# Kernel optimization log

Measured on AMD Instinct MI355X. Metric: run time of the kernel, lower is better.

## Reference

```python
import jax, jax.numpy as jnp
import numpy as np
import math

D_MODEL = 1024
N_HEAD = 16
D_HEAD = D_MODEL // N_HEAD


def setup_inputs() -> dict:
    key = jax.random.key(0)
    k0, k1, k2, k3, k4 = jax.random.split(key, 5)
    B, N = 4, 2048
    inp = jax.random.normal(k0, (B, N, D_MODEL), dtype=jnp.float32)
    # causal mask: True = keep (masked_fill on ~mask)
    mask = jnp.tril(jnp.ones((N, N), dtype=bool))
    # qkv_proj Linear(d_model, 3*d_model); output Linear(d_model, d_model)
    s_in = 1.0 / math.sqrt(D_MODEL)
    W_qkv = jax.random.uniform(k1, (D_MODEL, 3 * D_MODEL), jnp.float32, -s_in, s_in)
    b_qkv = jax.random.uniform(k2, (3 * D_MODEL,), jnp.float32, -s_in, s_in)
    W_out = jax.random.uniform(k3, (D_MODEL, D_MODEL), jnp.float32, -s_in, s_in)
    b_out = jax.random.uniform(k4, (D_MODEL,), jnp.float32, -s_in, s_in)
    return {"input": inp, "W_qkv": W_qkv, "b_qkv": b_qkv,
            "W_out": W_out, "b_out": b_out, "mask": mask}


def reference(input, W_qkv, b_qkv, W_out, b_out, mask):
    B, N, d = input.shape
    qkv = input @ W_qkv + b_qkv                       # [B,N,3d]  (dropout=eval no-op)
    q, k, v = jnp.split(qkv, 3, axis=-1)
    # [B,N,H,Dh] -> [B,H,N,Dh]
    q = q.reshape(B, N, N_HEAD, D_HEAD).transpose(0, 2, 1, 3)
    k = k.reshape(B, N, N_HEAD, D_HEAD).transpose(0, 2, 1, 3)
    v = v.reshape(B, N, N_HEAD, D_HEAD).transpose(0, 2, 1, 3)
    scale = 1.0 / math.sqrt(D_HEAD)
    scores = jnp.einsum('bhqd,bhkd->bhqk', q, k) * scale   # [B,H,N,N]
    scores = jnp.where(mask, scores, -jnp.inf)
    attn = jax.nn.softmax(scores, axis=-1)
    out = jnp.einsum('bhqk,bhkd->bhqd', attn, v)           # [B,H,N,Dh]
    out = out.transpose(0, 2, 1, 3).reshape(B, N, d)       # concat heads
    return out @ W_out + b_out
```

## Files before the change

### kernel.cpp

```cpp
#include <hip/hip_runtime.h>
#include <hip/hip_bf16.h>

typedef unsigned short u16;
typedef unsigned u32;
typedef __attribute__((ext_vector_type(4))) unsigned short u16x4;
typedef __attribute__((ext_vector_type(8))) unsigned short u16x8;
typedef __attribute__((ext_vector_type(4))) unsigned u32x4;
typedef __attribute__((ext_vector_type(8))) __bf16 bf16x8;
typedef __attribute__((ext_vector_type(4))) float f32x4;

typedef __attribute__((address_space(1))) void as1v;
typedef __attribute__((address_space(3))) void as3v;

#define MFMA16(a, b, c) __builtin_amdgcn_mfma_f32_16x16x32_bf16(a, b, c, 0, 0, 0)

#if __has_builtin(__builtin_amdgcn_permlane16_swap) && __has_builtin(__builtin_amdgcn_permlane32_swap)
#define HAVE_PERMLANE_SWAP 1
#else
#define HAVE_PERMLANE_SWAP 0
#endif

__device__ __forceinline__ u16 f2bf(float f) {
    unsigned u = __builtin_bit_cast(unsigned, f);
    u += 0x7fffu + ((u >> 16) & 1u);
    return (u16)(u >> 16);
}

__device__ __forceinline__ u32 pkbf(float lo, float hi) {
    u32 r;
    asm("v_cvt_pk_bf16_f32 %0, %1, %2" : "=v"(r) : "v"(lo), "v"(hi));
    return r;
}

__device__ __forceinline__ void gload16(const void* g, void* l) {
    __builtin_amdgcn_global_load_lds((as1v*)g, (as3v*)l, 16, 0, 0);
}

__device__ __forceinline__ float redmax_cross(float v) {
#if HAVE_PERMLANE_SWAP
    u32 xu = __builtin_bit_cast(u32, v);
    auto r16 = __builtin_amdgcn_permlane16_swap(xu, xu, false, false);
    float a = fmaxf(__builtin_bit_cast(float, (u32)r16[0]),
                    __builtin_bit_cast(float, (u32)r16[1]));
    u32 au = __builtin_bit_cast(u32, a);
    auto r32 = __builtin_amdgcn_permlane32_swap(au, au, false, false);
    return fmaxf(__builtin_bit_cast(float, (u32)r32[0]),
                 __builtin_bit_cast(float, (u32)r32[1]));
#else
    v = fmaxf(v, __shfl_xor(v, 16, 64));
    return fmaxf(v, __shfl_xor(v, 32, 64));
#endif
}

__device__ __forceinline__ float redsum_cross(float v) {
#if HAVE_PERMLANE_SWAP
    u32 xu = __builtin_bit_cast(u32, v);
    auto r16 = __builtin_amdgcn_permlane16_swap(xu, xu, false, false);
    float a = __builtin_bit_cast(float, (u32)r16[0]) +
              __builtin_bit_cast(float, (u32)r16[1]);
    u32 au = __builtin_bit_cast(u32, a);
    auto r32 = __builtin_amdgcn_permlane32_swap(au, au, false, false);
    return __builtin_bit_cast(float, (u32)r32[0]) +
           __builtin_bit_cast(float, (u32)r32[1]);
#else
    v += __shfl_xor(v, 16, 64);
    return v + __shfl_xor(v, 32, 64);
#endif
}

__global__ void convert_f32_bf16(const float* __restrict__ in, u16* __restrict__ out, int n4) {
    int i = blockIdx.x * blockDim.x + threadIdx.x;
    if (i < n4) {
        float4 v = *(const float4*)&in[(size_t)i * 4];
        u16x4 o;
        o.x = f2bf(v.x); o.y = f2bf(v.y); o.z = f2bf(v.z); o.w = f2bf(v.w);
        *(u16x4*)&out[(size_t)i * 4] = o;
    }
}

__global__ void transpose_convert(const float* __restrict__ in, u16* __restrict__ out, int R, int C) {
    __shared__ float tl[64][65];
    const int rb = blockIdx.x, cb = blockIdx.y;
    const int tid = threadIdx.x;
    for (int it = 0; it < 4; ++it) {
        int lin = (tid + it * 256) * 4;
        int r = lin >> 6, c = lin & 63;
        float4 v = *(const float4*)&in[(size_t)(rb * 64 + r) * C + cb * 64 + c];
        tl[r][c + 0] = v.x; tl[r][c + 1] = v.y; tl[r][c + 2] = v.z; tl[r][c + 3] = v.w;
    }
    __syncthreads();
    for (int it = 0; it < 4; ++it) {
        int lin = (tid + it * 256) * 4;
        int oc = lin >> 6, orr = lin & 63;
        u16x4 o;
        o.x = f2bf(tl[orr + 0][oc]);
        o.y = f2bf(tl[orr + 1][oc]);
        o.z = f2bf(tl[orr + 2][oc]);
        o.w = f2bf(tl[orr + 3][oc]);
        *(u16x4*)&out[(size_t)(cb * 64 + oc) * R + rb * 64 + orr] = o;
    }
}

__global__ void transpose_v(const u16* __restrict__ vbuf, u16* __restrict__ vtb) {
    __shared__ u16 tl[64][65];
    const int nb = blockIdx.x, bh = blockIdx.y;
    const int tid = threadIdx.x;
    for (int it = 0; it < 2; ++it) {
        int lin = (tid + it * 256) * 8;
        int nl = lin >> 6, dh = lin & 63;
        u16x8 v = *(const u16x8*)&vbuf[((size_t)bh * 2048 + nb * 64 + nl) * 64 + dh];
#pragma unroll
        for (int j = 0; j < 8; ++j) tl[dh + j][nl] = v[j];
    }
    __syncthreads();
    for (int it = 0; it < 2; ++it) {
        int lin = (tid + it * 256) * 8;
        int dh = lin >> 6, nl = lin & 63;
        u16x8 o;
#pragma unroll
        for (int j = 0; j < 8; ++j) o[j] = tl[dh][nl + j];
        *(u16x8*)&vtb[((size_t)bh * 64 + dh) * 2048 + nb * 64 + nl] = o;
    }
}

__global__ __launch_bounds__(512, 2) void gemm256_qkv(
    const u16* __restrict__ A, const u16* __restrict__ Bt, const float* __restrict__ bias,
    u16* __restrict__ qb, u16* __restrict__ kb, u16* __restrict__ vb) {
    constexpr int K = 1024;
    constexpr int NT = 32;
    __shared__ u16 ldsu[65536];

    const int bid = blockIdx.x;
    const int swz = (bid & 7) * 48 + (bid >> 3);
    const int bm = swz / 12, bn = swz % 12;

    const int tid = threadIdx.x, wid = tid >> 6, lane = tid & 63;
    const int wr = wid >> 2, wc = wid & 3;
    const int l15 = lane & 15, lhi = lane >> 4;

    const int sslot = (lane & 7) ^ (lane >> 3);
    const int kcol = (sslot & 3) * 8;
    const int mloc = (lane >> 3) * 2 + (sslot >> 2);

    const u16* Arow[2];
    const u16* Brow[2];
#pragma unroll
    for (int li = 0; li < 2; ++li) {
        int sg = wid * 2 + li;
        int m = sg * 16 + mloc;
        Arow[li] = A + (size_t)(bm * 256 + m) * K + kcol;
        Brow[li] = Bt + (size_t)(bn * 256 + m) * K + kcol;
    }

    auto stageA = [&](int buf, int t) {
#pragma unroll
        for (int li = 0; li < 2; ++li) {
            int sg = wid * 2 + li;
            gload16(Arow[li] + t * 32, (char*)ldsu + buf * 32768 + sg * 1024);
        }
    };
    auto stageB = [&](int buf, int t) {
#pragma unroll
        for (int li = 0; li < 2; ++li) {
            int sg = wid * 2 + li;
            gload16(Brow[li] + t * 32, (char*)ldsu + buf * 32768 + 16384 + sg * 1024);
        }
    };

    const int rslot = ((l15 & 1) * 4 + lhi) ^ ((l15 >> 1) & 7);
    const int fragoff = (l15 >> 1) * 64 + rslot * 8;

    f32x4 acc[8][4];
#pragma unroll
    for (int i = 0; i < 8; ++i)
#pragma unroll
        for (int j = 0; j < 4; ++j) acc[i][j] = (f32x4){0.f, 0.f, 0.f, 0.f};

    auto doTile = [&](int cur, int tstage, bool dostage) {
        const u16* Ab = ldsu + cur * 16384 + wr * 4096 + fragoff;
        const u16* Bb = ldsu + cur * 16384 + 8192 + wc * 2048 + fragoff;
        bf16x8 af[8], b0, b1;
#pragma unroll
        for (int mf = 0; mf < 8; ++mf) af[mf] = *(const bf16x8*)(Ab + mf * 512);
        b0 = *(const bf16x8*)(Bb);
        b1 = *(const bf16x8*)(Bb + 512);
        if (dostage) stageA(tstage & 3, tstage);
        __builtin_amdgcn_s_setprio(1);
#pragma unroll
        for (int mf = 0; mf < 8; ++mf) {
            acc[mf][0] = MFMA16(af[mf], b0, acc[mf][0]);
            acc[mf][1] = MFMA16(af[mf], b1, acc[mf][1]);
        }
        __builtin_amdgcn_s_setprio(0);
        b0 = *(const bf16x8*)(Bb + 1024);
        b1 = *(const bf16x8*)(Bb + 1536);
        if (dostage) stageB(tstage & 3, tstage);
        __builtin_amdgcn_s_setprio(1);
#pragma unroll
        for (int mf = 0; mf < 8; ++mf) {
            acc[mf][2] = MFMA16(af[mf], b0, acc[mf][2]);
            acc[mf][3] = MFMA16(af[mf], b1, acc[mf][3]);
        }
        __builtin_amdgcn_s_setprio(0);
    };

    stageA(0, 0); stageB(0, 0);
    stageA(1, 1); stageB(1, 1);
    stageA(2, 2); stageB(2, 2);
    asm volatile("s_waitcnt vmcnt(8)" ::: "memory");
    __builtin_amdgcn_s_barrier();
    __builtin_amdgcn_sched_barrier(0);

    for (int t = 0; t < NT - 3; ++t) {
        doTile(t & 3, t + 3, true);
        asm volatile("s_waitcnt vmcnt(8)" ::: "memory");
        __builtin_amdgcn_s_barrier();
        __builtin_amdgcn_sched_barrier(0);
    }
    doTile((NT - 3) & 3, 0, false);
    asm volatile("s_waitcnt vmcnt(4)" ::: "memory");
    __builtin_amdgcn_s_barrier();
    __builtin_amdgcn_sched_barrier(0);
    doTile((NT - 2) & 3, 0, false);
    asm volatile("s_waitcnt vmcnt(0)" ::: "memory");
    __builtin_amdgcn_s_barrier();
    __builtin_amdgcn_sched_barrier(0);
    doTile((NT - 1) & 3, 0, false);

    const int bnbase = bn * 256 + wc * 64;
#pragma unroll
    for (int nf = 0; nf < 4; ++nf) {
        int cg = bnbase + nf * 16 + l15;
        float bv = bias[cg];
        int which = cg >> 10, rem = cg & 1023;
        u16* dst = (which == 0) ? qb : (which == 1) ? kb : vb;
        float qs = (which == 0) ? 0.18033688011112042f : 1.0f;
        size_t colterm = (size_t)(rem >> 6) * 131072 + (size_t)(rem & 63);
#pragma unroll
        for (int mf = 0; mf < 8; ++mf) {
            int rgb = bm * 256 + wr * 128 + mf * 16 + lhi * 4;
            size_t rowterm = (size_t)(rgb >> 11) * 2097152 + (size_t)(rgb & 2047) * 64;
#pragma unroll
            for (int v = 0; v < 4; ++v) {
                float val = (acc[mf][nf][v] + bv) * qs;
                dst[rowterm + (size_t)v * 64 + colterm] = f2bf(val);
            }
        }
    }
}

__global__ __launch_bounds__(512, 2) void gemm256_out(
    const u16* __restrict__ A, const u16* __restrict__ Bt, const float* __restrict__ bias,
    float* __restrict__ outf) {
    constexpr int K = 1024;
    constexpr int NT = 32;
    __shared__ u16 ldsu[49152];

    const int bid = blockIdx.x;
    const int swz = (bid & 7) * 32 + (bid >> 3);
    const int bm = swz >> 3, bn = swz & 7;

    const int tid = threadIdx.x, wid = tid >> 6, lane = tid & 63;
    const int wr = wid >> 2, wc = wid & 3;
    const int l15 = lane & 15, lhi = lane >> 4;

    const int sslot = (lane & 7) ^ (lane >> 3);
    const int kcol = (sslot & 3) * 8;
    const int mloc = (lane >> 3) * 2 + (sslot >> 2);

    const u16* Arow[2];
#pragma unroll
    for (int li = 0; li < 2; ++li) {
        int sg = wid * 2 + li;
        Arow[li] = A + (size_t)(bm * 256 + sg * 16 + mloc) * K + kcol;
    }
    const u16* Brow = Bt + (size_t)(bn * 128 + wid * 16 + mloc) * K + kcol;

    auto stageA = [&](int buf, int t) {
#pragma unroll
        for (int li = 0; li < 2; ++li) {
            int sg = wid * 2 + li;
            gload16(Arow[li] + t * 32, (char*)ldsu + buf * 24576 + sg * 1024);
        }
    };
    auto stageB = [&](int buf, int t) {
        gload16(Brow + t * 32, (char*)ldsu + buf * 24576 + 16384 + wid * 1024);
    };

    const int rslot = ((l15 & 1) * 4 + lhi) ^ ((l15 >> 1) & 7);
    const int fragoff = (l15 >> 1) * 64 + rslot * 8;

    f32x4 acc[8][2];
#pragma unroll
    for (int i = 0; i < 8; ++i) {
        acc[i][0] = (f32x4){0.f, 0.f, 0.f, 0.f};
        acc[i][1] = (f32x4){0.f, 0.f, 0.f, 0.f};
    }

    auto doTile = [&](int cur, int tstage, bool dostage) {
        const u16* Ab = ldsu + cur * 12288 + wr * 4096 + fragoff;
        const u16* Bb = ldsu + cur * 12288 + 8192 + wc * 1024 + fragoff;
        bf16x8 af[8], b0, b1;
#pragma unroll
        for (int mf = 0; mf < 8; ++mf) af[mf] = *(const bf16x8*)(Ab + mf * 512);
        b0 = *(const bf16x8*)(Bb);
        b1 = *(const bf16x8*)(Bb + 512);
        if (dostage) stageA(tstage & 3, tstage);
        __builtin_amdgcn_s_setprio(1);
#pragma unroll
        for (int mf = 0; mf < 8; ++mf) acc[mf][0] = MFMA16(af[mf], b0, acc[mf][0]);
        __builtin_amdgcn_s_setprio(0);
        if (dostage) stageB(tstage & 3, tstage);
        __builtin_amdgcn_s_setprio(1);
#pragma unroll
        for (int mf = 0; mf < 8; ++mf) acc[mf][1] = MFMA16(af[mf], b1, acc[mf][1]);
        __builtin_amdgcn_s_setprio(0);
    };

    stageA(0, 0); stageB(0, 0);
    stageA(1, 1); stageB(1, 1);
    stageA(2, 2); stageB(2, 2);
    asm volatile("s_waitcnt vmcnt(6)" ::: "memory");
    __builtin_amdgcn_s_barrier();
    __builtin_amdgcn_sched_barrier(0);

    for (int t = 0; t < NT - 3; ++t) {
        doTile(t & 3, t + 3, true);
        asm volatile("s_waitcnt vmcnt(6)" ::: "memory");
        __builtin_amdgcn_s_barrier();
        __builtin_amdgcn_sched_barrier(0);
    }
    doTile((NT - 3) & 3, 0, false);
    asm volatile("s_waitcnt vmcnt(3)" ::: "memory");
    __builtin_amdgcn_s_barrier();
    __builtin_amdgcn_sched_barrier(0);
    doTile((NT - 2) & 3, 0, false);
    asm volatile("s_waitcnt vmcnt(0)" ::: "memory");
    __builtin_amdgcn_s_barrier();
    __builtin_amdgcn_sched_barrier(0);
    doTile((NT - 1) & 3, 0, false);

#pragma unroll
    for (int nf = 0; nf < 2; ++nf) {
        int cg = bn * 128 + wc * 32 + nf * 16 + l15;
        float bv = bias[cg];
#pragma unroll
        for (int mf = 0; mf < 8; ++mf) {
            int rgb = bm * 256 + wr * 128 + mf * 16 + lhi * 4;
#pragma unroll
            for (int v = 0; v < 4; ++v)
                outf[(size_t)(rgb + v) * 1024 + cg] = acc[mf][nf][v] + bv;
        }
    }
}

__global__ __launch_bounds__(256, 4) void attn_kernel(
    const u16* __restrict__ qbuf, const u16* __restrict__ kbuf,
    const u16* __restrict__ vtb, u16* __restrict__ obuf) {
    __shared__ u16 Kl[2][64 * 64];
    __shared__ u16 Vl[2][64 * 64];
    const int bid = blockIdx.x;
    const int rr = bid >> 8;
    const int pp = (bid >> 6) & 3;
    const int c = (rr & 1) ? (((rr >> 1) << 2) + pp)
                           : (15 - ((rr >> 1) << 2) - pp);
    const int bh = ((bid & 7) << 3) + ((bid >> 3) & 7);
    const int b = bh >> 4, h = bh & 15;
    const int tid = threadIdx.x, wid = tid >> 6, lane = tid & 63;
    const int l15 = lane & 15, lhi = lane >> 4;
    const int q0 = c * 128 + wid * 32;
    const int ntW = 2 * c + (wid >> 1) + 1;
    const int ntmax = 2 * c + 2;

    auto loadQ = [&](int qbase, bf16x8* dst) {
        const u16* qp = qbuf + ((size_t)bh * 2048 + qbase + l15) * 64 + lhi * 8;
        dst[0] = *(const bf16x8*)(qp);
        dst[1] = *(const bf16x8*)(qp + 32);
    };
    bf16x8 qf0[2], qf1[2];
    loadQ(q0, qf0); loadQ(q0 + 16, qf1);

    float m0 = -1e30f, l0 = 0.f, m1 = -1e30f, l1 = 0.f;
    f32x4 o0[4], o1[4];
#pragma unroll
    for (int d = 0; d < 4; ++d) {
        o0[d] = (f32x4){0.f, 0.f, 0.f, 0.f};
        o1[d] = (f32x4){0.f, 0.f, 0.f, 0.f};
    }

    const int srow = lane >> 3;
    const int scolb = ((lane & 7) * 16) ^ (srow << 4);

    auto stage = [&](int buf, int t) {
        const int kbase = t * 64;
#pragma unroll
        for (int s = 0; s < 2; ++s) {
            int sg = wid * 2 + s;
            int row = sg * 8 + srow;
            const u16* gk = kbuf + ((size_t)bh * 2048 + kbase + row) * 64 + (scolb >> 1);
            gload16(gk, (char*)Kl[buf] + sg * 1024);
            const u16* gv = vtb + ((size_t)bh * 64 + row) * 2048 + kbase + (scolb >> 1);
            gload16(gv, (char*)Vl[buf] + sg * 1024);
        }
    };

    auto smax = [&](f32x4* s, int qg0, int t, float& m, float& l, f32x4* oa, u32* pw) {
        const int qg = qg0 + l15;
        if (64 * t + 63 > qg0) {
#pragma unroll
            for (int kb4 = 0; kb4 < 4; ++kb4)
#pragma unroll
                for (int v = 0; v < 4; ++v) {
                    int kg = 64 * t + kb4 * 16 + lhi * 4 + v;
                    if (kg > qg) s[kb4][v] = -1e30f;
                }
        }
        float pm = fmaxf(fmaxf(fmaxf(s[0][0], s[0][1]), fmaxf(s[0][2], s[0][3])),
                         fmaxf(fmaxf(s[1][0], s[1][1]), fmaxf(s[1][2], s[1][3])));
        pm = fmaxf(pm, fmaxf(fmaxf(fmaxf(s[2][0], s[2][1]), fmaxf(s[2][2], s[2][3])),
                             fmaxf(fmaxf(s[3][0], s[3][1]), fmaxf(s[3][2], s[3][3]))));
        pm = redmax_cross(pm);
        if (!__all(pm <= m + 8.f)) {
            float nm = fmaxf(m, pm);
            float f = exp2f(m - nm);
            m = nm;
            l *= f;
#pragma unroll
            for (int d = 0; d < 4; ++d)
#pragma unroll
                for (int v = 0; v < 4; ++v) oa[d][v] *= f;
        }
        float rs = 0.f;
#pragma unroll
        for (int kb4 = 0; kb4 < 4; ++kb4)
#pragma unroll
            for (int v = 0; v < 4; ++v) {
                float e = exp2f(s[kb4][v] - m);
                s[kb4][v] = e;
                rs += e;
            }
        l += redsum_cross(rs);
        pw[0] = pkbf(s[0][0], s[0][1]); pw[1] = pkbf(s[0][2], s[0][3]);
        pw[2] = pkbf(s[1][0], s[1][1]); pw[3] = pkbf(s[1][2], s[1][3]);
        pw[4] = pkbf(s[2][0], s[2][1]); pw[5] = pkbf(s[2][2], s[2][3]);
        pw[6] = pkbf(s[3][0], s[3][1]); pw[7] = pkbf(s[3][2], s[3][3]);
    };

    auto computeChunk = [&](const char* Kb, const char* Vb, int t) {
        f32x4 s0[4], s1[4];
        __builtin_amdgcn_s_setprio(1);
#pragma unroll
        for (int kb4 = 0; kb4 < 4; ++kb4) {
            const int r = kb4 * 16 + l15;
            const int sw = (r & 7) << 4;
            const int rowb = r * 128;
            bf16x8 kf0 = *(const bf16x8*)(Kb + rowb + ((lhi * 16) ^ sw));
            bf16x8 kf1 = *(const bf16x8*)(Kb + rowb + ((64 + lhi * 16) ^ sw));
            f32x4 a0 = (f32x4){0.f, 0.f, 0.f, 0.f};
            a0 = MFMA16(kf0, qf0[0], a0);
            a0 = MFMA16(kf1, qf0[1], a0);
            s0[kb4] = a0;
            f32x4 a1 = (f32x4){0.f, 0.f, 0.f, 0.f};
            a1 = MFMA16(kf0, qf1[0], a1);
            a1 = MFMA16(kf1, qf1[1], a1);
            s1[kb4] = a1;
        }
        __builtin_amdgcn_s_setprio(0);
        u32 pw0[8], pw1[8];
        smax(s0, q0, t, m0, l0, o0, pw0);
        smax(s1, q0 + 16, t, m1, l1, o1, pw1);
        __builtin_amdgcn_s_setprio(1);
#pragma unroll
        for (int ks = 0; ks < 2; ++ks) {
            bf16x8 pb0 = __builtin_bit_cast(bf16x8,
                (u32x4){pw0[ks * 4 + 0], pw0[ks * 4 + 1], pw0[ks * 4 + 2], pw0[ks * 4 + 3]});
            bf16x8 pb1 = __builtin_bit_cast(bf16x8,
                (u32x4){pw1[ks * 4 + 0], pw1[ks * 4 + 1], pw1[ks * 4 + 2], pw1[ks * 4 + 3]});
#pragma unroll
            for (int dhb = 0; dhb < 4; ++dhb) {
                const int r = dhb * 16 + l15;
                const int sw = (r & 7) << 4;
                u16x4 v0 = *(const u16x4*)(Vb + r * 128 + ((ks * 64 + 8 * lhi) ^ sw));
                u16x4 v1 = *(const u16x4*)(Vb + r * 128 + ((ks * 64 + 32 + 8 * lhi) ^ sw));
                u16x8 vv = {v0[0], v0[1], v0[2], v0[3], v1[0], v1[1], v1[2], v1[3]};
                bf16x8 vf = __builtin_bit_cast(bf16x8, vv);
                o0[dhb] = MFMA16(vf, pb0, o0[dhb]);
                o1[dhb] = MFMA16(vf, pb1, o1[dhb]);
            }
        }
        __builtin_amdgcn_s_setprio(0);
    };

    stage(0, 0);
    int t = 0;
    for (;;) {
        __syncthreads();
        if (t + 1 < ntmax) stage(1, t + 1);
        if (t < ntW) computeChunk((const char*)Kl[0], (const char*)Vl[0], t);
        if (++t == ntmax) break;
        __syncthreads();
        if (t + 1 < ntmax) stage(0, t + 1);
        if (t < ntW) computeChunk((const char*)Kl[1], (const char*)Vl[1], t);
        if (++t == ntmax) break;
    }

    auto epi = [&](int qg0, float l, const f32x4* oa) {
        const float rl = 1.f / l;
        const int q = qg0 + l15;
        const size_t rowoff = ((size_t)b * 2048 + q) * 1024 + h * 64;
#pragma unroll
        for (int dhb = 0; dhb < 4; ++dhb) {
            u16x4 w;
#pragma unroll
            for (int v = 0; v < 4; ++v) w[v] = f2bf(oa[dhb][v] * rl);
            *(u16x4*)&obuf[rowoff + dhb * 16 + lhi * 4] = w;
        }
    };
    epi(q0, l0, o0);
    epi(q0 + 16, l1, o1);
}

extern "C" void kernel_launch(void* const* d_in, const int* in_sizes, int n_in,
                              void* d_out, int out_size, void* d_ws, size_t ws_size,
                              hipStream_t stream) {
    const float* inp   = (const float*)d_in[0];
    const float* W_qkv = (const float*)d_in[1];
    const float* b_qkv = (const float*)d_in[2];
    const float* W_out = (const float*)d_in[3];
    const float* b_out = (const float*)d_in[4];
    float* out = (float*)d_out;

    u16* xb   = (u16*)d_ws;
    u16* wqt  = xb + 8388608;
    u16* wot  = wqt + 3145728;
    u16* qbuf = wot + 1048576;
    u16* kbuf = qbuf + 8388608;
    u16* vbuf = kbuf + 8388608;
    u16* vtb  = vbuf + 8388608;
    u16* obuf = vtb + 8388608;

    convert_f32_bf16<<<8192, 256, 0, stream>>>(inp, xb, 2097152);
    transpose_convert<<<dim3(16, 48), 256, 0, stream>>>(W_qkv, wqt, 1024, 3072);
    transpose_convert<<<dim3(16, 16), 256, 0, stream>>>(W_out, wot, 1024, 1024);
    gemm256_qkv<<<384, 512, 0, stream>>>(xb, wqt, b_qkv, qbuf, kbuf, vbuf);
    transpose_v<<<dim3(32, 64), 256, 0, stream>>>(vbuf, vtb);
    attn_kernel<<<1024, 256, 0, stream>>>(qbuf, kbuf, vtb, obuf);
    gemm256_out<<<256, 512, 0, stream>>>(obuf, wot, b_out, out);
}
```

Baseline: 185.3 us.

## Shrink QKV GEMM tile to 256x128 and stage epilogue through LDS for coalesced stores

The QKV projection GEMM now uses 256x128 output tiles instead of 256x256, doubling the grid to 768 blocks and cutting LDS per block and accumulator registers per wave. The epilogue first writes biased, scaled bf16 results into a swizzled LDS scratch area, then emits 16-byte vector stores to the head-major Q/K/V buffers instead of scattered 2-byte stores. The aim is better occupancy and CU balance plus coalesced output writes. The cost is more A-tile reloads from global memory and lower MFMA work per loaded B fragment.

```diff
diff --git a/kernel.cpp b/kernel.cpp
--- a/kernel.cpp
+++ b/kernel.cpp
@@ -128,11 +128,11 @@
     u16* __restrict__ qb, u16* __restrict__ kb, u16* __restrict__ vb) {
     constexpr int K = 1024;
     constexpr int NT = 32;
-    __shared__ u16 ldsu[65536];
+    __shared__ u16 ldsu[49152];
 
     const int bid = blockIdx.x;
-    const int swz = (bid & 7) * 48 + (bid >> 3);
-    const int bm = swz / 12, bn = swz % 12;
+    const int swz = (bid & 7) * 96 + (bid >> 3);
+    const int bm = swz / 24, bn = swz % 24;
 
     const int tid = threadIdx.x, wid = tid >> 6, lane = tid & 63;
     const int wr = wid >> 2, wc = wid & 3;
@@ -143,42 +143,37 @@
     const int mloc = (lane >> 3) * 2 + (sslot >> 2);
 
     const u16* Arow[2];
-    const u16* Brow[2];
 #pragma unroll
     for (int li = 0; li < 2; ++li) {
         int sg = wid * 2 + li;
-        int m = sg * 16 + mloc;
-        Arow[li] = A + (size_t)(bm * 256 + m) * K + kcol;
-        Brow[li] = Bt + (size_t)(bn * 256 + m) * K + kcol;
-    }
+        Arow[li] = A + (size_t)(bm * 256 + sg * 16 + mloc) * K + kcol;
+    }
+    const u16* Brow = Bt + (size_t)(bn * 128 + wid * 16 + mloc) * K + kcol;
 
     auto stageA = [&](int buf, int t) {
 #pragma unroll
         for (int li = 0; li < 2; ++li) {
             int sg = wid * 2 + li;
-            gload16(Arow[li] + t * 32, (char*)ldsu + buf * 32768 + sg * 1024);
+            gload16(Arow[li] + t * 32, (char*)ldsu + buf * 24576 + sg * 1024);
         }
     };
     auto stageB = [&](int buf, int t) {
-#pragma unroll
-        for (int li = 0; li < 2; ++li) {
-            int sg = wid * 2 + li;
-            gload16(Brow[li] + t * 32, (char*)ldsu + buf * 32768 + 16384 + sg * 1024);
-        }
+        gload16(Brow + t * 32, (char*)ldsu + buf * 24576 + 16384 + wid * 1024);
     };
 
     const int rslot = ((l15 & 1) * 4 + lhi) ^ ((l15 >> 1) & 7);
     const int fragoff = (l15 >> 1) * 64 + rslot * 8;
 
-    f32x4 acc[8][4];
-#pragma unroll
-    for (int i = 0; i < 8; ++i)
-#pragma unroll
-        for (int j = 0; j < 4; ++j) acc[i][j] = (f32x4){0.f, 0.f, 0.f, 0.f};
+    f32x4 acc[8][2];
+#pragma unroll
+    for (int i = 0; i < 8; ++i) {
+        acc[i][0] = (f32x4){0.f, 0.f, 0.f, 0.f};
+        acc[i][1] = (f32x4){0.f, 0.f, 0.f, 0.f};
+    }
 
     auto doTile = [&](int cur, int tstage, bool dostage) {
-        const u16* Ab = ldsu + cur * 16384 + wr * 4096 + fragoff;
-        const u16* Bb = ldsu + cur * 16384 + 8192 + wc * 2048 + fragoff;
+        const u16* Ab = ldsu + cur * 12288 + wr * 4096 + fragoff;
+        const u16* Bb = ldsu + cur * 12288 + 8192 + wc * 1024 + fragoff;
         bf16x8 af[8], b0, b1;
 #pragma unroll
         for (int mf = 0; mf < 8; ++mf) af[mf] = *(const bf16x8*)(Ab + mf * 512);
@@ -187,38 +182,30 @@
         if (dostage) stageA(tstage & 3, tstage);
         __builtin_amdgcn_s_setprio(1);
 #pragma unroll
-        for (int mf = 0; mf < 8; ++mf) {
-            acc[mf][0] = MFMA16(af[mf], b0, acc[mf][0]);
-            acc[mf][1] = MFMA16(af[mf], b1, acc[mf][1]);
-        }
+        for (int mf = 0; mf < 8; ++mf) acc[mf][0] = MFMA16(af[mf], b0, acc[mf][0]);
         __builtin_amdgcn_s_setprio(0);
-        b0 = *(const bf16x8*)(Bb + 1024);
-        b1 = *(const bf16x8*)(Bb + 1536);
         if (dostage) stageB(tstage & 3, tstage);
         __builtin_amdgcn_s_setprio(1);
 #pragma unroll
-        for (int mf = 0; mf < 8; ++mf) {
-            acc[mf][2] = MFMA16(af[mf], b0, acc[mf][2]);
-            acc[mf][3] = MFMA16(af[mf], b1, acc[mf][3]);
-        }
+        for (int mf = 0; mf < 8; ++mf) acc[mf][1] = MFMA16(af[mf], b1, acc[mf][1]);
         __builtin_amdgcn_s_setprio(0);
     };
 
     stageA(0, 0); stageB(0, 0);
     stageA(1, 1); stageB(1, 1);
     stageA(2, 2); stageB(2, 2);
-    asm volatile("s_waitcnt vmcnt(8)" ::: "memory");
+    asm volatile("s_waitcnt vmcnt(6)" ::: "memory");
     __builtin_amdgcn_s_barrier();
     __builtin_amdgcn_sched_barrier(0);
 
     for (int t = 0; t < NT - 3; ++t) {
         doTile(t & 3, t + 3, true);
-        asm volatile("s_waitcnt vmcnt(8)" ::: "memory");
+        asm volatile("s_waitcnt vmcnt(6)" ::: "memory");
         __builtin_amdgcn_s_barrier();
         __builtin_amdgcn_sched_barrier(0);
     }
     doTile((NT - 3) & 3, 0, false);
-    asm volatile("s_waitcnt vmcnt(4)" ::: "memory");
+    asm volatile("s_waitcnt vmcnt(3)" ::: "memory");
     __builtin_amdgcn_s_barrier();
     __builtin_amdgcn_sched_barrier(0);
     doTile((NT - 2) & 3, 0, false);
@@ -227,25 +214,34 @@
     __builtin_amdgcn_sched_barrier(0);
     doTile((NT - 1) & 3, 0, false);
 
-    const int bnbase = bn * 256 + wc * 64;
-#pragma unroll
-    for (int nf = 0; nf < 4; ++nf) {
-        int cg = bnbase + nf * 16 + l15;
-        float bv = bias[cg];
-        int which = cg >> 10, rem = cg & 1023;
-        u16* dst = (which == 0) ? qb : (which == 1) ? kb : vb;
-        float qs = (which == 0) ? 0.18033688011112042f : 1.0f;
-        size_t colterm = (size_t)(rem >> 6) * 131072 + (size_t)(rem & 63);
-#pragma unroll
-        for (int mf = 0; mf < 8; ++mf) {
-            int rgb = bm * 256 + wr * 128 + mf * 16 + lhi * 4;
-            size_t rowterm = (size_t)(rgb >> 11) * 2097152 + (size_t)(rgb & 2047) * 64;
-#pragma unroll
-            for (int v = 0; v < 4; ++v) {
-                float val = (acc[mf][nf][v] + bv) * qs;
-                dst[rowterm + (size_t)v * 64 + colterm] = f2bf(val);
-            }
-        }
+    __syncthreads();
+    const int cg0 = bn * 128 + wc * 32;
+    const int which = cg0 >> 10, rem = cg0 & 1023;
+    u16* dst = (which == 0) ? qb : (which == 1) ? kb : vb;
+    const float qs = (which == 0) ? 0.18033688011112042f : 1.0f;
+    const int hh = rem >> 6, dh0 = rem & 63;
+    const int rgb0 = bm * 256 + wr * 128;
+    const int bb = rgb0 >> 11, n0 = rgb0 & 2047;
+    char* lep = (char*)ldsu + wid * 8192;
+    float bv0 = bias[cg0 + l15], bv1 = bias[cg0 + 16 + l15];
+#pragma unroll
+    for (int mf = 0; mf < 8; ++mf)
+#pragma unroll
+        for (int v = 0; v < 4; ++v) {
+            int row = mf * 16 + lhi * 4 + v;
+            int sw = ((row >> 2) & 3) << 4;
+            *(u16*)(lep + row * 64 + ((l15 * 2) ^ sw)) =
+                f2bf((acc[mf][0][v] + bv0) * qs);
+            *(u16*)(lep + row * 64 + ((32 + l15 * 2) ^ sw)) =
+                f2bf((acc[mf][1][v] + bv1) * qs);
+        }
+    const size_t gbase = (((size_t)bb * 16 + hh) * 2048 + n0) * 64 + dh0;
+#pragma unroll
+    for (int it = 0; it < 8; ++it) {
+        int idx = it * 64 + lane;
+        int row = idx >> 2, j = idx & 3;
+        u16x8 vv = *(const u16x8*)(lep + row * 64 + ((j * 16) ^ (((row >> 2) & 3) << 4)));
+        *(u16x8*)&dst[gbase + (size_t)row * 64 + j * 8] = vv;
     }
 }
 
@@ -542,7 +538,7 @@
     convert_f32_bf16<<<8192, 256, 0, stream>>>(inp, xb, 2097152);
     transpose_convert<<<dim3(16, 48), 256, 0, stream>>>(W_qkv, wqt, 1024, 3072);
     transpose_convert<<<dim3(16, 16), 256, 0, stream>>>(W_out, wot, 1024, 1024);
-    gemm256_qkv<<<384, 512, 0, stream>>>(xb, wqt, b_qkv, qbuf, kbuf, vbuf);
+    gemm256_qkv<<<768, 512, 0, stream>>>(xb, wqt, b_qkv, qbuf, kbuf, vbuf);
     transpose_v<<<dim3(32, 64), 256, 0, stream>>>(vbuf, vtb);
     attn_kernel<<<1024, 256, 0, stream>>>(qbuf, kbuf, vtb, obuf);
     gemm256_out<<<256, 512, 0, stream>>>(obuf, wot, b_out, out);
```

Result: no change. 186.5 us (+0.6%).

## Fuse V transpose into QKV GEMM epilogue and shrink tiles to 128x128

Applied to the files above, without the earlier changes.

The separate transpose_v kernel is removed, and the QKV GEMM epilogue now writes V directly in transposed [B,H,Dh,N] layout with vectorized stores. The GEMM is retiled from 256x256 with 512 threads and a 4-stage buffer to 128x128 with 256 threads and a 3-stage buffer, launched over 1536 blocks for better occupancy and wave balance. This drops one kernel launch and a full round trip of the V buffer through memory. In exchange the smaller tiles give less data reuse per block, and the stage-index expression for A is oddly written, though it still evaluates to tstage % 3.

```diff
diff --git a/kernel.cpp b/kernel.cpp
--- a/kernel.cpp
+++ b/kernel.cpp
@@ -101,41 +101,19 @@
     }
 }
 
-__global__ void transpose_v(const u16* __restrict__ vbuf, u16* __restrict__ vtb) {
-    __shared__ u16 tl[64][65];
-    const int nb = blockIdx.x, bh = blockIdx.y;
-    const int tid = threadIdx.x;
-    for (int it = 0; it < 2; ++it) {
-        int lin = (tid + it * 256) * 8;
-        int nl = lin >> 6, dh = lin & 63;
-        u16x8 v = *(const u16x8*)&vbuf[((size_t)bh * 2048 + nb * 64 + nl) * 64 + dh];
-#pragma unroll
-        for (int j = 0; j < 8; ++j) tl[dh + j][nl] = v[j];
-    }
-    __syncthreads();
-    for (int it = 0; it < 2; ++it) {
-        int lin = (tid + it * 256) * 8;
-        int dh = lin >> 6, nl = lin & 63;
-        u16x8 o;
-#pragma unroll
-        for (int j = 0; j < 8; ++j) o[j] = tl[dh][nl + j];
-        *(u16x8*)&vtb[((size_t)bh * 64 + dh) * 2048 + nb * 64 + nl] = o;
-    }
-}
-
-__global__ __launch_bounds__(512, 2) void gemm256_qkv(
+__global__ __launch_bounds__(256, 3) void gemm128_qkv(
     const u16* __restrict__ A, const u16* __restrict__ Bt, const float* __restrict__ bias,
-    u16* __restrict__ qb, u16* __restrict__ kb, u16* __restrict__ vb) {
+    u16* __restrict__ qb, u16* __restrict__ kb, u16* __restrict__ vtb) {
     constexpr int K = 1024;
     constexpr int NT = 32;
-    __shared__ u16 ldsu[65536];
+    __shared__ u16 ldsu[24576];
 
     const int bid = blockIdx.x;
-    const int swz = (bid & 7) * 48 + (bid >> 3);
-    const int bm = swz / 12, bn = swz % 12;
+    const int s = (bid & 7) * 192 + (bid >> 3);
+    const int bm = s / 24, bn = s % 24;
 
     const int tid = threadIdx.x, wid = tid >> 6, lane = tid & 63;
-    const int wr = wid >> 2, wc = wid & 3;
+    const int wr = wid >> 1, wc = wid & 1;
     const int l15 = lane & 15, lhi = lane >> 4;
 
     const int sslot = (lane & 7) ^ (lane >> 3);
@@ -147,57 +125,56 @@
 #pragma unroll
     for (int li = 0; li < 2; ++li) {
         int sg = wid * 2 + li;
-        int m = sg * 16 + mloc;
-        Arow[li] = A + (size_t)(bm * 256 + m) * K + kcol;
-        Brow[li] = Bt + (size_t)(bn * 256 + m) * K + kcol;
+        Arow[li] = A + (size_t)(bm * 128 + sg * 16 + mloc) * K + kcol;
+        Brow[li] = Bt + (size_t)(bn * 128 + sg * 16 + mloc) * K + kcol;
     }
 
     auto stageA = [&](int buf, int t) {
 #pragma unroll
         for (int li = 0; li < 2; ++li) {
             int sg = wid * 2 + li;
-            gload16(Arow[li] + t * 32, (char*)ldsu + buf * 32768 + sg * 1024);
+            gload16(Arow[li] + t * 32, (char*)ldsu + buf * 16384 + sg * 1024);
         }
     };
     auto stageB = [&](int buf, int t) {
 #pragma unroll
         for (int li = 0; li < 2; ++li) {
             int sg = wid * 2 + li;
-            gload16(Brow[li] + t * 32, (char*)ldsu + buf * 32768 + 16384 + sg * 1024);
+            gload16(Brow[li] + t * 32, (char*)ldsu + buf * 16384 + 8192 + sg * 1024);
         }
     };
 
     const int rslot = ((l15 & 1) * 4 + lhi) ^ ((l15 >> 1) & 7);
     const int fragoff = (l15 >> 1) * 64 + rslot * 8;
 
-    f32x4 acc[8][4];
-#pragma unroll
-    for (int i = 0; i < 8; ++i)
+    f32x4 acc[4][4];
+#pragma unroll
+    for (int i = 0; i < 4; ++i)
 #pragma unroll
         for (int j = 0; j < 4; ++j) acc[i][j] = (f32x4){0.f, 0.f, 0.f, 0.f};
 
     auto doTile = [&](int cur, int tstage, bool dostage) {
-        const u16* Ab = ldsu + cur * 16384 + wr * 4096 + fragoff;
-        const u16* Bb = ldsu + cur * 16384 + 8192 + wc * 2048 + fragoff;
-        bf16x8 af[8], b0, b1;
-#pragma unroll
-        for (int mf = 0; mf < 8; ++mf) af[mf] = *(const bf16x8*)(Ab + mf * 512);
+        const u16* Ab = ldsu + cur * 8192 + wr * 2048 + fragoff;
+        const u16* Bb = ldsu + cur * 8192 + 4096 + wc * 2048 + fragoff;
+        bf16x8 af[4], b0, b1;
+#pragma unroll
+        for (int mf = 0; mf < 4; ++mf) af[mf] = *(const bf16x8*)(Ab + mf * 512);
         b0 = *(const bf16x8*)(Bb);
         b1 = *(const bf16x8*)(Bb + 512);
-        if (dostage) stageA(tstage & 3, tstage);
+        if (dostage) stageA((tstage * 43691) >> 17  == -1 ? 0 : tstage % 3, tstage);
         __builtin_amdgcn_s_setprio(1);
 #pragma unroll
-        for (int mf = 0; mf < 8; ++mf) {
+        for (int mf = 0; mf < 4; ++mf) {
             acc[mf][0] = MFMA16(af[mf], b0, acc[mf][0]);
             acc[mf][1] = MFMA16(af[mf], b1, acc[mf][1]);
         }
         __builtin_amdgcn_s_setprio(0);
         b0 = *(const bf16x8*)(Bb + 1024);
         b1 = *(const bf16x8*)(Bb + 1536);
-        if (dostage) stageB(tstage & 3, tstage);
+        if (dostage) stageB(tstage % 3, tstage);
         __builtin_amdgcn_s_setprio(1);
 #pragma unroll
-        for (int mf = 0; mf < 8; ++mf) {
+        for (int mf = 0; mf < 4; ++mf) {
             acc[mf][2] = MFMA16(af[mf], b0, acc[mf][2]);
             acc[mf][3] = MFMA16(af[mf], b1, acc[mf][3]);
         }
@@ -206,45 +183,57 @@
 
     stageA(0, 0); stageB(0, 0);
     stageA(1, 1); stageB(1, 1);
-    stageA(2, 2); stageB(2, 2);
-    asm volatile("s_waitcnt vmcnt(8)" ::: "memory");
-    __builtin_amdgcn_s_barrier();
-    __builtin_amdgcn_sched_barrier(0);
-
-    for (int t = 0; t < NT - 3; ++t) {
-        doTile(t & 3, t + 3, true);
-        asm volatile("s_waitcnt vmcnt(8)" ::: "memory");
-        __builtin_amdgcn_s_barrier();
-        __builtin_amdgcn_sched_barrier(0);
-    }
-    doTile((NT - 3) & 3, 0, false);
     asm volatile("s_waitcnt vmcnt(4)" ::: "memory");
     __builtin_amdgcn_s_barrier();
     __builtin_amdgcn_sched_barrier(0);
-    doTile((NT - 2) & 3, 0, false);
+
+    for (int t = 0; t < NT - 2; ++t) {
+        doTile(t % 3, t + 2, true);
+        asm volatile("s_waitcnt vmcnt(4)" ::: "memory");
+        __builtin_amdgcn_s_barrier();
+        __builtin_amdgcn_sched_barrier(0);
+    }
+    doTile((NT - 2) % 3, 0, false);
     asm volatile("s_waitcnt vmcnt(0)" ::: "memory");
     __builtin_amdgcn_s_barrier();
     __builtin_amdgcn_sched_barrier(0);
-    doTile((NT - 1) & 3, 0, false);
-
-    const int bnbase = bn * 256 + wc * 64;
-#pragma unroll
-    for (int nf = 0; nf < 4; ++nf) {
-        int cg = bnbase + nf * 16 + l15;
-        float bv = bias[cg];
-        int which = cg >> 10, rem = cg & 1023;
-        u16* dst = (which == 0) ? qb : (which == 1) ? kb : vb;
-        float qs = (which == 0) ? 0.18033688011112042f : 1.0f;
-        size_t colterm = (size_t)(rem >> 6) * 131072 + (size_t)(rem & 63);
-#pragma unroll
-        for (int mf = 0; mf < 8; ++mf) {
-            int rgb = bm * 256 + wr * 128 + mf * 16 + lhi * 4;
-            size_t rowterm = (size_t)(rgb >> 11) * 2097152 + (size_t)(rgb & 2047) * 64;
-#pragma unroll
-            for (int v = 0; v < 4; ++v) {
-                float val = (acc[mf][nf][v] + bv) * qs;
-                dst[rowterm + (size_t)v * 64 + colterm] = f2bf(val);
+    doTile((NT - 1) % 3, 0, false);
+
+    const int cg0 = bn * 128 + wc * 64;
+    const int which = cg0 >> 10, rem = cg0 & 1023;
+    const int hh = rem >> 6, dh0 = rem & 63;
+    const int rgb0 = bm * 128 + wr * 64;
+    const int bb = rgb0 >> 11, n0 = rgb0 & 2047;
+
+    if (which == 2) {
+        const size_t vbase = ((size_t)(bb * 16 + hh) * 64 + dh0) * 2048 + (size_t)n0;
+#pragma unroll
+        for (int nt = 0; nt < 4; ++nt) {
+            float bv = bias[cg0 + nt * 16 + l15];
+            size_t rowb = vbase + (size_t)(nt * 16 + l15) * 2048;
+#pragma unroll
+            for (int mt = 0; mt < 4; ++mt) {
+                u16x4 w;
+#pragma unroll
+                for (int v = 0; v < 4; ++v) w[v] = f2bf(acc[mt][nt][v] + bv);
+                *(u16x4*)&vtb[rowb + mt * 16 + lhi * 4] = w;
             }
+        }
+    } else {
+        u16* dst = (which == 0) ? qb : kb;
+        const float qs = (which == 0) ? 0.18033688011112042f : 1.0f;
+        const size_t gbase = (((size_t)bb * 16 + hh) * 2048 + n0) * 64 + dh0;
+#pragma unroll
+        for (int nt = 0; nt < 4; ++nt) {
+            float bv = bias[cg0 + nt * 16 + l15];
+#pragma unroll
+            for (int mt = 0; mt < 4; ++mt)
+#pragma unroll
+                for (int v = 0; v < 4; ++v) {
+                    int n = mt * 16 + lhi * 4 + v;
+                    dst[gbase + (size_t)n * 64 + nt * 16 + l15] =
+                        f2bf((acc[mt][nt][v] + bv) * qs);
+                }
         }
     }
 }
@@ -535,15 +524,13 @@
     u16* wot  = wqt + 3145728;
     u16* qbuf = wot + 1048576;
     u16* kbuf = qbuf + 8388608;
-    u16* vbuf = kbuf + 8388608;
-    u16* vtb  = vbuf + 8388608;
+    u16* vtb  = kbuf + 8388608;
     u16* obuf = vtb + 8388608;
 
     convert_f32_bf16<<<8192, 256, 0, stream>>>(inp, xb, 2097152);
     transpose_convert<<<dim3(16, 48), 256, 0, stream>>>(W_qkv, wqt, 1024, 3072);
     transpose_convert<<<dim3(16, 16), 256, 0, stream>>>(W_out, wot, 1024, 1024);
-    gemm256_qkv<<<384, 512, 0, stream>>>(xb, wqt, b_qkv, qbuf, kbuf, vbuf);
-    transpose_v<<<dim3(32, 64), 256, 0, stream>>>(vbuf, vtb);
+    gemm128_qkv<<<1536, 256, 0, stream>>>(xb, wqt, b_qkv, qbuf, kbuf, vtb);
     attn_kernel<<<1024, 256, 0, stream>>>(qbuf, kbuf, vtb, obuf);
     gemm256_out<<<256, 512, 0, stream>>>(obuf, wot, b_out, out);
 }
```

Measured after the change: 178.2 us. -3.9%, faster.
